# Kernel optimization log

Hardware: AMD Instinct MI355X
Metric: run time of the kernel (lower is better)

Reference implementation:

```python
import jax, jax.numpy as jnp
import numpy as np

B, NS, NT = 8, 1024, 1024
SRC, TGT, OUT, H = 1024, 1024, 1024, 8
DH = OUT // H  # per-head dim = 128


def setup_inputs() -> dict:
    key = jax.random.key(0)
    ks = jax.random.split(key, 9)
    s = 0.02
    return {
        "src": jax.random.normal(ks[0], (B, NS, SRC), jnp.float32),
        "tgt": jax.random.normal(ks[1], (B, NT, TGT), jnp.float32),
        "src_mask": jnp.ones((B, NS), jnp.float32),
        "tgt_mask": jnp.ones((B, NT), jnp.float32),
        "Ws": jax.random.normal(ks[2], (2 * OUT, SRC), jnp.float32) * s,
        "bs": jnp.zeros((2 * OUT,), jnp.float32),
        "Wt": jax.random.normal(ks[3], (OUT, TGT), jnp.float32) * s,
        "bt": jnp.zeros((OUT,), jnp.float32),
        "Wo": jax.random.normal(ks[4], (OUT, OUT + TGT), jnp.float32) * s,
        "bo": jnp.zeros((OUT,), jnp.float32),
    }


def reference(src, tgt, src_mask, tgt_mask, Ws, bs, Wt, bt, Wo, bo):
    # src_lin / tgt_lin (FCNet = linear, no activation, drop=0 at eval)
    src_trans = jnp.einsum("bsf,of->bso", src, Ws) + bs  # [B,NS,2*OUT]
    tgt_trans = jnp.einsum("btf,of->bto", tgt, Wt) + bt  # [B,NT,OUT]
    src_trans = src_trans * src_mask[:, :, None]
    tgt_trans = tgt_trans * tgt_mask[:, :, None]

    src_key, src_val = jnp.split(src_trans, 2, axis=2)  # each [B,NS,OUT]
    # head split along channels == reshape to [.., H, DH]
    k = src_key.reshape(B, NS, H, DH)
    v = src_val.reshape(B, NS, H, DH)
    q = tgt_trans.reshape(B, NT, H, DH)

    scores = jnp.einsum("bthd,bshd->bhts", q, k) / jnp.sqrt(jnp.float32(DH))
    scores = jnp.where(src_mask[:, None, None, :] == 0, -jnp.inf, scores)
    attn = jax.nn.softmax(scores, axis=-1)  # [B,H,NT,NS]
    tgt_update = jnp.einsum("bhts,bshd->bthd", attn, v).reshape(B, NT, OUT)

    cat_tgt = jnp.concatenate([tgt, tgt_update], axis=2)  # [B,NT,TGT+OUT]
    update_tgt = jnp.einsum("btf,of->bto", cat_tgt, Wo) + bo
    return update_tgt
```

## Files before the change

kernel.cpp:

```cpp
#include <hip/hip_runtime.h>


typedef __bf16 bf16x8 __attribute__((ext_vector_type(8)));
typedef float f32x4 __attribute__((ext_vector_type(4)));
typedef unsigned short u16;
typedef unsigned short u16x8 __attribute__((ext_vector_type(8)));

#define MFMA16(a, b, c) __builtin_amdgcn_mfma_f32_16x16x32_bf16((a), (b), (c), 0, 0, 0)

__device__ __forceinline__ float bf2f(u16 b) {
  return __uint_as_float(((unsigned)b) << 16);
}
__device__ __forceinline__ u16 f2bf(float f) {
  unsigned u = __float_as_uint(f);
  u += 0x7fffu + ((u >> 16) & 1u);
  return (u16)(u >> 16);
}
__device__ __forceinline__ u16 f2bf_hw(float f) {
  __bf16 h = (__bf16)f;
  return __builtin_bit_cast(u16, h);
}

__device__ __forceinline__ void async16(const u16* g, u16* l) {
  __builtin_amdgcn_global_load_lds(
      (const __attribute__((address_space(1))) unsigned int*)g,
      (__attribute__((address_space(3))) unsigned int*)l, 16, 0, 0);
}

struct Cvt5 {
  const float* src[5];
  unsigned cnt4[5];
  unsigned ooff[5];
};

__global__ __launch_bounds__(256)
void cvt5_kernel(Cvt5 a, u16* __restrict__ out, unsigned total4)
{
  unsigned gid = blockIdx.x * 256u + threadIdx.x;
  if (gid >= total4) return;
  unsigned rem = gid;
  int s = 0;
  while (s < 4 && rem >= a.cnt4[s]) { rem -= a.cnt4[s]; ++s; }
  const float4 v = ((const float4*)a.src[s])[rem];
  ushort4 o;
  o.x = f2bf(v.x); o.y = f2bf(v.y); o.z = f2bf(v.z); o.w = f2bf(v.w);
  *(ushort4*)(out + a.ooff[s] + (size_t)rem * 4) = o;
}

__global__ __launch_bounds__(256, 3)
void gemm12_kernel(const u16* __restrict__ srcb, const u16* __restrict__ tgtb,
                   const u16* __restrict__ Wsb, const u16* __restrict__ Wtb,
                   const float* __restrict__ bs, const float* __restrict__ bt,
                   const float* __restrict__ smask, const float* __restrict__ tmask,
                   u16* __restrict__ kvbuf, u16* __restrict__ qbuf)
{
  __shared__ u16 smem[16384];
  u16* As = smem;
  u16* Bs = smem + 8192;

  const int tid  = threadIdx.x;
  const int lane = tid & 63;
  const int w    = tid >> 6;
  const int wm = w >> 1, wn = w & 1;
  const int quad = lane >> 4, lr = lane & 15;

  const unsigned nwg  = gridDim.x * gridDim.y;
  const unsigned wgid = blockIdx.y * gridDim.x + blockIdx.x;
  const unsigned swz  = (wgid & 7u) * (nwg >> 3) + (wgid >> 3);
  const int nt = (int)(swz % gridDim.x);
  const int mt = (int)(swz / gridDim.x);
  const int m0 = mt * 128;
  const int n0 = nt * 128;

  const bool isQ = (n0 >= 2048);
  const u16* Ap = isQ ? tgtb : srcb;
  const u16* Bp = isQ ? (Wtb + (size_t)(n0 - 2048) * 1024)
                      : (Wsb + (size_t)n0 * 1024);
  const float* bias = isQ ? (bt + (n0 - 2048)) : (bs + n0);
  const float* rsc  = isQ ? tmask : smask;

  const f32x4 z4 = {0.f, 0.f, 0.f, 0.f};
  f32x4 acc[4][4];
#pragma unroll
  for (int i = 0; i < 4; ++i)
#pragma unroll
    for (int j = 0; j < 4; ++j)
      acc[i][j] = z4;

  const int acolsw = (((tid & 7) ^ ((tid >> 3) & 7)) * 8);
  const int ssw = lr & 7;

  for (int k0 = 0; k0 < 1024; k0 += 64) {
    __syncthreads();
#pragma unroll
    for (int it = 0; it < 4; ++it) {
      const int row = it * 32 + (tid >> 3);
      const int ldsbase = (it * 256 + (tid & 192)) * 8;
      async16(Ap + (size_t)(m0 + row) * 1024 + (k0 + acolsw), &As[ldsbase]);
      async16(Bp + (size_t)row * 1024        + (k0 + acolsw), &Bs[ldsbase]);
    }
    __syncthreads();

#pragma unroll
    for (int kk = 0; kk < 2; ++kk) {
      const int rc = (((kk << 2) | quad) ^ ssw) * 8;
      bf16x8 af[4], bfr[4];
#pragma unroll
      for (int i = 0; i < 4; ++i)
        af[i] = *(const bf16x8*)&As[(wm * 64 + i * 16 + lr) * 64 + rc];
#pragma unroll
      for (int j = 0; j < 4; ++j)
        bfr[j] = *(const bf16x8*)&Bs[(wn * 64 + j * 16 + lr) * 64 + rc];
#pragma unroll
      for (int i = 0; i < 4; ++i)
#pragma unroll
        for (int j = 0; j < 4; ++j)
          acc[i][j] = MFMA16(af[i], bfr[j], acc[i][j]);
    }
  }

  float bv[4];
#pragma unroll
  for (int j = 0; j < 4; ++j)
    bv[j] = bias[wn * 64 + j * 16 + lr];

  if (isQ) {
    const int c0 = n0 - 2048;
#pragma unroll
    for (int i = 0; i < 4; ++i)
#pragma unroll
      for (int r = 0; r < 4; ++r) {
        const int grow = m0 + wm * 64 + i * 16 + quad * 4 + r;
        const float rs = rsc[grow];
#pragma unroll
        for (int j = 0; j < 4; ++j) {
          const int gcol = c0 + wn * 64 + j * 16 + lr;
          qbuf[(size_t)grow * 1024 + gcol] = f2bf_hw((acc[i][j][r] + bv[j]) * rs);
        }
      }
  } else {
    u16* kvtile = smem;
    __syncthreads();

    const int bb  = m0 >> 10;
    const int s0b = m0 & 1023;
    const bool isK = (n0 < 1024);
    const int h = (isK ? n0 : n0 - 1024) >> 7;
    const size_t bh = (size_t)(bb * 8 + h);

#pragma unroll
    for (int i = 0; i < 4; ++i)
#pragma unroll
      for (int r = 0; r < 4; ++r) {
        const int sl = wm * 64 + i * 16 + quad * 4 + r;
        const float rs = rsc[m0 + sl];
#pragma unroll
        for (int j = 0; j < 4; ++j) {
          const int d = wn * 64 + j * 16 + lr;
          const float val = (acc[i][j][r] + bv[j]) * rs;
          int c, e;
          if (isK) {
            c = (d >> 3) * 128 + sl;
            c ^= ((c >> 2) & 2) ^ ((c >> 7) & 1);
            e = d & 7;
          } else {
            c = (sl >> 6) * 1024 + (((sl >> 3) & 7) * 128) + d;
            c ^= (c >> 7) & 1;
            e = sl & 7;
          }
          kvtile[c * 8 + e] = f2bf_hw(val);
        }
      }
    __syncthreads();

    const size_t gbase = isK
        ? (bh * 131072 + (size_t)s0b * 8)
        : ((size_t)8388608 + bh * 131072 + (size_t)(s0b >> 6) * 8192);
#pragma unroll
    for (int it = 0; it < 8; ++it) {
      const int idx = it * 256 + tid;
      int lc;
      size_t dst;
      if (isK) {
        lc  = idx ^ ((idx >> 2) & 2) ^ ((idx >> 7) & 1);
        dst = gbase + (size_t)(idx >> 7) * 8192 + (size_t)(idx & 127) * 8;
      } else {
        lc  = idx ^ ((idx >> 7) & 1);
        dst = gbase + (size_t)idx * 8;
      }
      *(u16x8*)(kvbuf + dst) = *(const u16x8*)&kvtile[lc * 8];
    }
  }
}

__global__ __launch_bounds__(256, 3)
void gemm3_kernel(const u16* __restrict__ A0, const u16* __restrict__ A1,
                  const u16* __restrict__ Bw, const float* __restrict__ bias,
                  float* __restrict__ C)
{
  __shared__ u16 As[128 * 64];
  __shared__ u16 Bs[128 * 64];
  const int tid  = threadIdx.x;
  const int lane = tid & 63;
  const int w    = tid >> 6;
  const int wm = w >> 1, wn = w & 1;
  const int quad = lane >> 4, lr = lane & 15;
  const unsigned nwg  = gridDim.x * gridDim.y;
  const unsigned wgid = blockIdx.y * gridDim.x + blockIdx.x;
  const unsigned swz  = (wgid & 7u) * (nwg >> 3) + (wgid >> 3);
  const int m0 = (int)(swz / gridDim.x) * 128;
  const int n0 = (int)(swz % gridDim.x) * 128;

  const f32x4 z4 = {0.f, 0.f, 0.f, 0.f};
  f32x4 acc[4][4];
#pragma unroll
  for (int i = 0; i < 4; ++i)
#pragma unroll
    for (int j = 0; j < 4; ++j)
      acc[i][j] = z4;

  const int acolsw = (((tid & 7) ^ ((tid >> 3) & 7)) * 8);
  const int ssw = lr & 15 & 7;

  auto kstep = [&](const u16* Ap, int kk0, int k0) {
    __syncthreads();
#pragma unroll
    for (int it = 0; it < 4; ++it) {
      const int row = it * 32 + (tid >> 3);
      const int ldsbase = (it * 256 + (tid & 192)) * 8;
      async16(Ap + (size_t)(m0 + row) * 1024 + (kk0 + acolsw), &As[ldsbase]);
      async16(Bw + (size_t)(n0 + row) * 2048 + (k0 + acolsw), &Bs[ldsbase]);
    }
    __syncthreads();

#pragma unroll
    for (int kk = 0; kk < 2; ++kk) {
      const int rc = (((kk << 2) | quad) ^ ssw) * 8;
      bf16x8 af[4], bfr[4];
#pragma unroll
      for (int i = 0; i < 4; ++i)
        af[i] = *(const bf16x8*)&As[(wm * 64 + i * 16 + lr) * 64 + rc];
#pragma unroll
      for (int j = 0; j < 4; ++j)
        bfr[j] = *(const bf16x8*)&Bs[(wn * 64 + j * 16 + lr) * 64 + rc];
#pragma unroll
      for (int i = 0; i < 4; ++i)
#pragma unroll
        for (int j = 0; j < 4; ++j)
          acc[i][j] = MFMA16(af[i], bfr[j], acc[i][j]);
    }
  };

  for (int k0 = 0; k0 < 1024; k0 += 64) kstep(A0, k0, k0);
  for (int k0 = 1024; k0 < 2048; k0 += 64) kstep(A1, k0 - 1024, k0);

  float bv[4];
#pragma unroll
  for (int j = 0; j < 4; ++j)
    bv[j] = bias[n0 + wn * 64 + j * 16 + lr];

#pragma unroll
  for (int i = 0; i < 4; ++i)
#pragma unroll
    for (int r = 0; r < 4; ++r) {
      const int grow = m0 + wm * 64 + i * 16 + quad * 4 + r;
#pragma unroll
      for (int j = 0; j < 4; ++j) {
        const int gcol = n0 + wn * 64 + j * 16 + lr;
        C[(size_t)grow * 1024 + gcol] = acc[i][j][r] + bv[j];
      }
    }
}

#define SCLOG2E 0.12751813754618667f

__global__ __launch_bounds__(256, 2)
void flash_kernel(const u16* __restrict__ q, const u16* __restrict__ Kg,
                  const u16* __restrict__ Vg,
                  const float* __restrict__ smask, u16* __restrict__ upd)
{
  __shared__ u16 Ks[64 * 128];
  __shared__ u16 Vs[64 * 128];
  __shared__ u16 Ps[4][2 * 16 * 64];

  const int tid  = threadIdx.x;
  const int lane = tid & 63;
  const int w    = tid >> 6;
  const int quad = lane >> 4, lr = lane & 15;
  const int bh_i = blockIdx.x;
  const int qt   = blockIdx.y;
  const int b = bh_i >> 3, h = bh_i & 7;
  const size_t bh = (size_t)bh_i;

  const size_t qrow0 = (size_t)b * 1024 + qt * 128 + w * 16;

  bf16x8 qf[2][4];
#pragma unroll
  for (int s = 0; s < 2; ++s)
#pragma unroll
    for (int kk = 0; kk < 4; ++kk)
      qf[s][kk] = *(const bf16x8*)
          &q[(qrow0 + s * 64 + lr) * 1024 + h * 128 + kk * 32 + quad * 8];

  const f32x4 z4 = {0.f, 0.f, 0.f, 0.f};
  f32x4 oacc[2][8];
#pragma unroll
  for (int s = 0; s < 2; ++s)
#pragma unroll
    for (int jd = 0; jd < 8; ++jd) oacc[s][jd] = z4;
  float lsum[2][4] = {{0.f, 0.f, 0.f, 0.f}, {0.f, 0.f, 0.f, 0.f}};

  for (int s0 = 0; s0 < 1024; s0 += 64) {
    const int t = s0 >> 6;
    __syncthreads();
#pragma unroll
    for (int it = 0; it < 4; ++it) {
      const int dc = it * 4 + w;
      async16(Kg + (((bh * 16 + dc) * 1024) + s0 + lane) * 8,
              &Ks[(it * 256 + (tid & 192)) * 8]);
    }
#pragma unroll
    for (int it = 0; it < 4; ++it) {
      const int f = it * 256 + tid;
      async16(Vg + ((bh * 16 + t) * 1024 + f) * 8,
              &Vs[(it * 256 + (tid & 192)) * 8]);
    }
    __syncthreads();

    f32x4 sacc[2][4];
#pragma unroll
    for (int s = 0; s < 2; ++s)
#pragma unroll
      for (int j = 0; j < 4; ++j) sacc[s][j] = z4;
    __builtin_amdgcn_s_setprio(1);
#pragma unroll
    for (int kk = 0; kk < 4; ++kk) {
      bf16x8 kb[4];
#pragma unroll
      for (int j = 0; j < 4; ++j)
        kb[j] = *(const bf16x8*)&Ks[((kk * 4 + quad) * 64 + j * 16 + lr) * 8];
#pragma unroll
      for (int s = 0; s < 2; ++s)
#pragma unroll
        for (int j = 0; j < 4; ++j)
          sacc[s][j] = MFMA16(qf[s][kk], kb[j], sacc[s][j]);
    }
    __builtin_amdgcn_s_setprio(0);

    float mb[4];
#pragma unroll
    for (int j = 0; j < 4; ++j) {
      const float mv = smask[b * 1024 + s0 + j * 16 + lr];
      mb[j] = (mv == 0.f) ? -1e30f : 0.f;
    }

#pragma unroll
    for (int s = 0; s < 2; ++s)
#pragma unroll
      for (int r = 0; r < 4; ++r) {
        const int row = quad * 4 + r;
        const int rsw = (row & 7) * 8;
        float ps = 0.f;
#pragma unroll
        for (int j = 0; j < 4; ++j) {
          const float p = exp2f(fmaf(sacc[s][j][r], SCLOG2E, mb[j]));
          ps += p;
          Ps[w][s * 1024 + row * 64 + ((j * 16 + lr) ^ rsw)] = f2bf_hw(p);
        }
        lsum[s][r] += ps;
      }

    __builtin_amdgcn_s_setprio(1);
#pragma unroll
    for (int kk2 = 0; kk2 < 2; ++kk2) {
      bf16x8 pa[2], vb[8];
#pragma unroll
      for (int s = 0; s < 2; ++s)
        pa[s] = *(const bf16x8*)
            &Ps[w][s * 1024 + lr * 64 + ((kk2 * 32 + quad * 8) ^ ((lr & 7) * 8))];
#pragma unroll
      for (int jd = 0; jd < 8; ++jd)
        vb[jd] = *(const bf16x8*)&Vs[((kk2 * 4 + quad) * 128 + jd * 16 + lr) * 8];
#pragma unroll
      for (int s = 0; s < 2; ++s)
#pragma unroll
        for (int jd = 0; jd < 8; ++jd)
          oacc[s][jd] = MFMA16(pa[s], vb[jd], oacc[s][jd]);
    }
    __builtin_amdgcn_s_setprio(0);
  }

#pragma unroll
  for (int s = 0; s < 2; ++s)
#pragma unroll
    for (int r = 0; r < 4; ++r) {
      float l = lsum[s][r];
      l += __shfl_xor(l, 1);
      l += __shfl_xor(l, 2);
      l += __shfl_xor(l, 4);
      l += __shfl_xor(l, 8);
      const float inv = 1.f / l;
      const size_t grow = qrow0 + s * 64 + quad * 4 + r;
#pragma unroll
      for (int jd = 0; jd < 8; ++jd)
        upd[grow * 1024 + h * 128 + jd * 16 + lr] = f2bf_hw(oacc[s][jd][r] * inv);
    }
}

__global__ void magic_kernel(float* out, float val)
{
  if (threadIdx.x == 0 && blockIdx.x == 0) out[0] = val;
}

extern "C" void kernel_launch(void* const* d_in, const int* in_sizes, int n_in,
                              void* d_out, int out_size, void* d_ws, size_t ws_size,
                              hipStream_t stream)
{
  static const int dict_sz[10]   = {8388608, 8388608, 8192, 8192, 2097152,
                                    2048, 1048576, 1024, 2097152, 1024};
  static const int sorted_sz[10] = {2097152, 2097152, 1048576, 1024, 2048,
                                    1024, 8388608, 8192, 8388608, 8192};
  bool is_dict = (n_in == 10), is_sorted = (n_in == 10);
  if (n_in == 10) {
    for (int i = 0; i < 10; ++i) {
      if (in_sizes[i] != dict_sz[i])   is_dict = false;
      if (in_sizes[i] != sorted_sz[i]) is_sorted = false;
    }
  }

  const float *src, *tgt, *smask, *tmask, *Ws, *bs, *Wt, *bt, *Wo, *bo;
  if (is_sorted) {
    Wo    = (const float*)d_in[0];
    Ws    = (const float*)d_in[1];
    Wt    = (const float*)d_in[2];
    bo    = (const float*)d_in[3];
    bs    = (const float*)d_in[4];
    bt    = (const float*)d_in[5];
    src   = (const float*)d_in[6];
    smask = (const float*)d_in[7];
    tgt   = (const float*)d_in[8];
    tmask = (const float*)d_in[9];
  } else {
    src   = (const float*)d_in[0];
    tgt   = (const float*)d_in[1];
    smask = (const float*)d_in[2];
    tmask = (const float*)d_in[3];
    Ws    = (const float*)d_in[4];
    bs    = (const float*)d_in[5];
    Wt    = (const float*)d_in[6];
    bt    = (const float*)d_in[7];
    Wo    = (const float*)d_in[8];
    bo    = (const float*)d_in[9];
  }
  float* out = (float*)d_out;

  const size_t KV = 16777216, Q = 8388608, UPD = 8388608;
  const unsigned segsz[5] = {8388608u, 8388608u, 2097152u, 1048576u, 2097152u};
  size_t total_u16 = KV + Q + UPD;
  unsigned aoff[5], off = 0, total4 = 0;
  for (int i = 0; i < 5; ++i) {
    aoff[i] = off;
    off += segsz[i];
    total4 += segsz[i] / 4u;
  }
  total_u16 += off;

  unsigned ws_mb = (unsigned)(ws_size >> 20);
  if (ws_mb > 999u) ws_mb = 999u;
  if (!is_dict && !is_sorted) {
    magic_kernel<<<dim3(1), dim3(64), 0, stream>>>(out, 4000.f + (float)ws_mb);
    return;
  }
  if (ws_size < total_u16 * 2) {
    magic_kernel<<<dim3(1), dim3(64), 0, stream>>>(out, 3000.f + (float)ws_mb);
    return;
  }

  u16* kvbuf  = (u16*)d_ws;
  u16* qbuf   = kvbuf + KV;
  u16* updbuf = qbuf + Q;
  u16* arena  = updbuf + UPD;

  Cvt5 ca;
  const float* segp[5] = {src, tgt, Ws, Wt, Wo};
  for (int i = 0; i < 5; ++i) {
    ca.src[i]  = segp[i];
    ca.cnt4[i] = segsz[i] / 4u;
    ca.ooff[i] = aoff[i];
  }
  const u16* srcb = arena + aoff[0];
  const u16* tgtb = arena + aoff[1];
  const u16* Wsb  = arena + aoff[2];
  const u16* Wtb  = arena + aoff[3];
  const u16* Wob  = arena + aoff[4];

  dim3 blk(256);
  cvt5_kernel<<<dim3((total4 + 255u) / 256u), blk, 0, stream>>>(ca, arena, total4);
  gemm12_kernel<<<dim3(24, 64), blk, 0, stream>>>(
      srcb, tgtb, Wsb, Wtb, bs, bt, smask, tmask, kvbuf, qbuf);
  flash_kernel<<<dim3(64, 8), blk, 0, stream>>>(
      qbuf, kvbuf, kvbuf + 8388608, smask, updbuf);
  gemm3_kernel<<<dim3(8, 64), blk, 0, stream>>>(
      tgtb, updbuf, Wob, bo, out);
}
```

Before: 300.5 us.

## Double-buffer K/V tiles in flash kernel with async prefetch two ahead

Splits the K and V shared-memory tiles into two buffers and issues async loads for tile t+2 while tile t is being computed. A vmcnt wait plus a raw barrier replaces the two syncthreads per iteration. The source mask is read once into a 64-bit bitmask before the loop instead of being loaded from global memory on every tile. LDS use doubles for K/V, which may lower occupancy below the declared 2 blocks per CU. The wrapped prefetch at the end loads redundant tiles that are never used.

```diff
diff --git a/kernel.cpp b/kernel.cpp
--- a/kernel.cpp
+++ b/kernel.cpp
@@ -220,7 +220,7 @@
       acc[i][j] = z4;
 
   const int acolsw = (((tid & 7) ^ ((tid >> 3) & 7)) * 8);
-  const int ssw = lr & 15 & 7;
+  const int ssw = lr & 7;
 
   auto kstep = [&](const u16* Ap, int kk0, int k0) {
     __syncthreads();
@@ -279,8 +279,8 @@
                   const u16* __restrict__ Vg,
                   const float* __restrict__ smask, u16* __restrict__ upd)
 {
-  __shared__ u16 Ks[64 * 128];
-  __shared__ u16 Vs[64 * 128];
+  __shared__ u16 Ks[2][64 * 128];
+  __shared__ u16 Vs[2][64 * 128];
   __shared__ u16 Ps[4][2 * 16 * 64];
 
   const int tid  = threadIdx.x;
@@ -302,30 +302,51 @@
       qf[s][kk] = *(const bf16x8*)
           &q[(qrow0 + s * 64 + lr) * 1024 + h * 128 + kk * 32 + quad * 8];
 
-  const f32x4 z4 = {0.f, 0.f, 0.f, 0.f};
-  f32x4 oacc[2][8];
-#pragma unroll
-  for (int s = 0; s < 2; ++s)
-#pragma unroll
-    for (int jd = 0; jd < 8; ++jd) oacc[s][jd] = z4;
-  float lsum[2][4] = {{0.f, 0.f, 0.f, 0.f}, {0.f, 0.f, 0.f, 0.f}};
-
-  for (int s0 = 0; s0 < 1024; s0 += 64) {
-    const int t = s0 >> 6;
-    __syncthreads();
+  unsigned long long mbits = 0ull;
+#pragma unroll
+  for (int t = 0; t < 16; ++t)
+#pragma unroll
+    for (int j = 0; j < 4; ++j) {
+      const float mv = smask[b * 1024 + t * 64 + j * 16 + lr];
+      if (mv == 0.f) mbits |= (1ull << (t * 4 + j));
+    }
+
+  auto stage = [&](int t, int bb) {
+    const int s0 = t * 64;
 #pragma unroll
     for (int it = 0; it < 4; ++it) {
       const int dc = it * 4 + w;
       async16(Kg + (((bh * 16 + dc) * 1024) + s0 + lane) * 8,
-              &Ks[(it * 256 + (tid & 192)) * 8]);
+              &Ks[bb][(it * 256 + (tid & 192)) * 8]);
     }
 #pragma unroll
     for (int it = 0; it < 4; ++it) {
-      const int f = it * 256 + tid;
-      async16(Vg + ((bh * 16 + t) * 1024 + f) * 8,
-              &Vs[(it * 256 + (tid & 192)) * 8]);
-    }
-    __syncthreads();
+      async16(Vg + ((bh * 16 + t) * 1024 + it * 256 + tid) * 8,
+              &Vs[bb][(it * 256 + (tid & 192)) * 8]);
+    }
+  };
+
+  const f32x4 z4 = {0.f, 0.f, 0.f, 0.f};
+  f32x4 oacc[2][8];
+#pragma unroll
+  for (int s = 0; s < 2; ++s)
+#pragma unroll
+    for (int jd = 0; jd < 8; ++jd) oacc[s][jd] = z4;
+  float lsum[2][4] = {{0.f, 0.f, 0.f, 0.f}, {0.f, 0.f, 0.f, 0.f}};
+
+  stage(0, 0);
+  stage(1, 1);
+
+#pragma unroll 1
+  for (int t = 0; t < 16; ++t) {
+    const int bb = t & 1;
+    asm volatile("s_waitcnt vmcnt(8)" ::: "memory");
+    __builtin_amdgcn_s_barrier();
+
+    float mb[4];
+#pragma unroll
+    for (int j = 0; j < 4; ++j)
+      mb[j] = ((mbits >> (t * 4 + j)) & 1ull) ? -1e30f : 0.f;
 
     f32x4 sacc[2][4];
 #pragma unroll
@@ -338,7 +359,7 @@
       bf16x8 kb[4];
 #pragma unroll
       for (int j = 0; j < 4; ++j)
-        kb[j] = *(const bf16x8*)&Ks[((kk * 4 + quad) * 64 + j * 16 + lr) * 8];
+        kb[j] = *(const bf16x8*)&Ks[bb][((kk * 4 + quad) * 64 + j * 16 + lr) * 8];
 #pragma unroll
       for (int s = 0; s < 2; ++s)
 #pragma unroll
@@ -346,13 +367,6 @@
           sacc[s][j] = MFMA16(qf[s][kk], kb[j], sacc[s][j]);
     }
     __builtin_amdgcn_s_setprio(0);
-
-    float mb[4];
-#pragma unroll
-    for (int j = 0; j < 4; ++j) {
-      const float mv = smask[b * 1024 + s0 + j * 16 + lr];
-      mb[j] = (mv == 0.f) ? -1e30f : 0.f;
-    }
 
 #pragma unroll
     for (int s = 0; s < 2; ++s)
@@ -380,7 +394,7 @@
             &Ps[w][s * 1024 + lr * 64 + ((kk2 * 32 + quad * 8) ^ ((lr & 7) * 8))];
 #pragma unroll
       for (int jd = 0; jd < 8; ++jd)
-        vb[jd] = *(const bf16x8*)&Vs[((kk2 * 4 + quad) * 128 + jd * 16 + lr) * 8];
+        vb[jd] = *(const bf16x8*)&Vs[bb][((kk2 * 4 + quad) * 128 + jd * 16 + lr) * 8];
 #pragma unroll
       for (int s = 0; s < 2; ++s)
 #pragma unroll
@@ -388,7 +402,12 @@
           oacc[s][jd] = MFMA16(pa[s], vb[jd], oacc[s][jd]);
     }
     __builtin_amdgcn_s_setprio(0);
-  }
+
+    __builtin_amdgcn_s_barrier();
+    stage((t + 2) & 15, bb);
+  }
+
+  asm volatile("s_waitcnt vmcnt(0)" ::: "memory");
 
 #pragma unroll
   for (int s = 0; s < 2; ++s)
```

Result: no change. 300.8 us (+0.1%).
